# Kernel tuning notes

Hardware: AMD Instinct MI355X
Metric: run time of the kernel (lower is better)

The kernel has to match this reference:

```python
import jax, jax.numpy as jnp
import numpy as np

DIM = 1024


def setup_inputs() -> dict:
    key = jax.random.key(0)
    k1, k2, k3, k4 = jax.random.split(key, 4)
    B, T, S, D = 32, 512, 1024, DIM
    inp = {
        "input": jax.random.normal(k1, (B, T, D), dtype=jnp.float32),
        "context": jax.random.normal(k2, (B, S, D), dtype=jnp.float32),
        # linear_in: nn.Linear(dim, dim, bias=False) -> weight [D, D]
        "W_in": jax.random.normal(k3, (D, D), dtype=jnp.float32) / np.sqrt(D),
        # linear_out: nn.Linear(2*dim, dim, bias=False for 'general') -> weight [D, 2D]
        "W_out": jax.random.normal(k4, (D, 2 * D), dtype=jnp.float32) / np.sqrt(2 * D),
    }
    return inp


def reference(input, context, W_in, W_out):
    # score: general -> h_t = linear_in(input); align = bmm(h_t, context^T)
    h_t = jnp.einsum("btd,ed->bte", input, W_in)              # [B,T,D]
    align = jnp.einsum("btd,bsd->bts", h_t, context)          # [B,T,S]
    align_vectors = jax.nn.softmax(align, axis=-1)            # [B,T,S]
    c = jnp.einsum("bts,bsd->btd", align_vectors, context)    # [B,T,D]
    concat_c = jnp.concatenate([c, input], axis=2)            # [B,T,2D]
    attn_h = jnp.tanh(jnp.einsum("btf,df->btd", concat_c, W_out))  # [B,T,D]
    # multi-step path: transpose to (tgt_len, batch, ...)
    attn_h = jnp.transpose(attn_h, (1, 0, 2))
    concat_c = jnp.transpose(concat_c, (1, 0, 2))
    align_vectors = jnp.transpose(align_vectors, (1, 0, 2))
    return attn_h, align_vectors, concat_c
```

## Files before the change

### kernel.cpp

```cpp
#include <hip/hip_runtime.h>
#include <cmath>

#define BATCH 32
#define TLEN  512
#define SLEN  1024
#define DIM   1024

#define BM 128
#define BN 128
#define BK2 64

typedef _Float16 h8 __attribute__((ext_vector_type(8)));
typedef _Float16 h4 __attribute__((ext_vector_type(4)));
typedef _Float16 h2 __attribute__((ext_vector_type(2)));
typedef float f4 __attribute__((ext_vector_type(4)));


__device__ __forceinline__ void gload16(const _Float16* g, _Float16* l) {
  __builtin_amdgcn_global_load_lds(
      (const __attribute__((address_space(1))) unsigned int*)g,
      (__attribute__((address_space(3))) unsigned int*)l, 16, 0, 0);
}

template <int EPI>
__global__ __launch_bounds__(256) void gemm16(
    const _Float16* __restrict__ A, const _Float16* __restrict__ Bm,
    float* __restrict__ C, _Float16* __restrict__ C16, int K,
    long lda, long ldb, long ldc, long ldc16,
    long strideA, long strideB, long strideC, long strideC16,
    const float* __restrict__ Xin) {
  __shared__ _Float16 As[BM * BK2];
  __shared__ _Float16 Bs[BM * BK2];

  const int bz = blockIdx.z;
  A += (long)bz * strideA;
  Bm += (long)bz * strideB;

  const int m0 = blockIdx.y * BM;
  const int n0 = blockIdx.x * BN;
  const int tid = threadIdx.x;
  const int lane = tid & 63;
  const int wave = tid >> 6;
  const int q = lane >> 4;
  const int r = lane & 15;
  const int wm = (wave >> 1) * 64;
  const int wn = (wave & 1) * 64;

  f4 acc[4][4];
#pragma unroll
  for (int i = 0; i < 4; ++i)
#pragma unroll
    for (int j = 0; j < 4; ++j) acc[i][j] = (f4){0.f, 0.f, 0.f, 0.f};

  const _Float16* gA[4];
  const _Float16* gB[4];
  _Float16* lA[4];
  _Float16* lB[4];
#pragma unroll
  for (int i = 0; i < 4; ++i) {
    const int c = i * 256 + tid;
    const int row = c >> 3;
    const int j = (c & 7) ^ (row & 7);
    gA[i] = A + (long)(m0 + row) * lda + j * 8;
    gB[i] = Bm + (long)(n0 + row) * ldb + j * 8;
    lA[i] = As + i * 2048 + wave * 512;
    lB[i] = Bs + i * 2048 + wave * 512;
  }

  for (int k0 = 0; k0 < K; k0 += BK2) {
#pragma unroll
    for (int i = 0; i < 4; ++i) gload16(gA[i] + k0, lA[i]);
#pragma unroll
    for (int i = 0; i < 4; ++i) gload16(gB[i] + k0, lB[i]);
    __syncthreads();

#pragma unroll
    for (int kk = 0; kk < 2; ++kk) {
      h8 av[4], bv[4];
#pragma unroll
      for (int mt = 0; mt < 4; ++mt) {
        const int row = wm + mt * 16 + r;
        const int u = (kk * 4 + q) ^ (r & 7);
        av[mt] = *(const h8*)&As[row * BK2 + u * 8];
      }
#pragma unroll
      for (int nt = 0; nt < 4; ++nt) {
        const int row = wn + nt * 16 + r;
        const int u = (kk * 4 + q) ^ (r & 7);
        bv[nt] = *(const h8*)&Bs[row * BK2 + u * 8];
      }
#pragma unroll
      for (int mt = 0; mt < 4; ++mt)
#pragma unroll
        for (int nt = 0; nt < 4; ++nt)
          acc[mt][nt] = __builtin_amdgcn_mfma_f32_16x16x32_f16(
              av[mt], bv[nt], acc[mt][nt], 0, 0, 0);
    }
    __syncthreads();
  }

#pragma unroll
  for (int mt = 0; mt < 4; ++mt) {
#pragma unroll
    for (int nt = 0; nt < 4; ++nt) {
#pragma unroll
      for (int i = 0; i < 4; ++i) {
        float x = acc[mt][nt][i];
        const long row = m0 + wm + mt * 16 + q * 4 + i;
        const long col = n0 + wn + nt * 16 + r;
        if constexpr (EPI == 1) x = tanhf(x);
        if constexpr (EPI != 2)
          C[(long)bz * strideC + row * ldc + col] = x;
        if constexpr (EPI >= 2)
          C16[(long)bz * strideC16 + row * ldc16 + col] = (_Float16)x;
      }
    }
  }

  if constexpr (EPI == 4) {
#pragma unroll
    for (int it = 0; it < 16; ++it) {
      const int idx = it * 256 + tid;
      const int row = idx >> 5;
      const int c4 = (idx & 31) * 4;
      const f4 v = *(const f4*)(Xin + ((long)bz * TLEN + m0 + row) * DIM +
                                n0 + c4);
      const long off = (long)bz * strideC + (long)(m0 + row) * ldc + DIM +
                       n0 + c4;
      *(f4*)(C + off) = v;
      h4 hv = {(_Float16)v.x, (_Float16)v.y, (_Float16)v.z, (_Float16)v.w};
      *(h4*)(C16 + (long)bz * strideC16 + (long)(m0 + row) * ldc16 + DIM +
             n0 + c4) = hv;
    }
  }
}

__global__ __launch_bounds__(256) void cvt3(
    const float* __restrict__ in, _Float16* __restrict__ out,
    const float* __restrict__ in2, _Float16* __restrict__ out2,
    const float* __restrict__ in3, _Float16* __restrict__ out3) {
  const int b = blockIdx.x;
  const float* src;
  _Float16* dst;
  long n;
  int b0, nb;
  if (b < 384) { src = in;  dst = out;  n = 16777216; b0 = 0;   nb = 384; }
  else if (b < 408) { src = in2; dst = out2; n = 1048576; b0 = 384; nb = 24; }
  else { src = in3; dst = out3; n = 2097152; b0 = 408; nb = 48; }
  long i = ((long)(b - b0) * 256 + threadIdx.x) * 4;
  const long stride = (long)nb * 1024;
  for (; i < n; i += stride) {
    f4 v = *(const f4*)(src + i);
    h4 hv = {(_Float16)v.x, (_Float16)v.y, (_Float16)v.z, (_Float16)v.w};
    *(h4*)(dst + i) = hv;
  }
}

#define CTPAD 68
__global__ __launch_bounds__(256) void ctx_cvt(
    const float* __restrict__ ctx, _Float16* __restrict__ c16,
    _Float16* __restrict__ c16t) {
  __shared__ _Float16 tile[64 * CTPAD];
  const int b = blockIdx.z;
  const int s0 = blockIdx.y * 64;
  const int d0 = blockIdx.x * 64;
  const int tr = threadIdx.x >> 4;
  const int tc = (threadIdx.x & 15) * 4;
#pragma unroll
  for (int i = 0; i < 4; ++i) {
    const int s = i * 16 + tr;
    float4 v = *(const float4*)(ctx + ((long)b * SLEN + s0 + s) * DIM + d0 + tc);
    h4 hv = {(_Float16)v.x, (_Float16)v.y, (_Float16)v.z, (_Float16)v.w};
    *(h4*)(c16 + ((long)b * SLEN + s0 + s) * DIM + d0 + tc) = hv;
    *(h4*)&tile[s * CTPAD + tc] = hv;
  }
  __syncthreads();
#pragma unroll
  for (int i = 0; i < 4; ++i) {
    const int d = i * 16 + tr;
    h4 hv = {tile[tc * CTPAD + d], tile[(tc + 1) * CTPAD + d],
             tile[(tc + 2) * CTPAD + d], tile[(tc + 3) * CTPAD + d]};
    *(h4*)(c16t + ((long)b * DIM + d0 + d) * SLEN + s0 + tc) = hv;
  }
}


#define AS_LD 40
#define B2_LD 134
#define BKF 32

template <bool B_IS_NT, bool TANH>
__global__ __launch_bounds__(256) void gemm_f16(
    const float* __restrict__ A, const float* __restrict__ Bm,
    float* __restrict__ C, int M, int N, int K, long lda, long ldb, long ldc,
    long strideA, long strideB, long strideC) {
  __shared__ _Float16 As[BM * AS_LD];
  __shared__ _Float16 Bs[BM * AS_LD];

  const int bz = blockIdx.z;
  A += (long)bz * strideA;
  Bm += (long)bz * strideB;
  C += (long)bz * strideC;

  const int m0 = blockIdx.y * BM;
  const int n0 = blockIdx.x * BN;
  const int tid = threadIdx.x;
  const int lane = tid & 63;
  const int wave = tid >> 6;
  const int wm = (wave >> 1) * 64;
  const int wn = (wave & 1) * 64;
  const int q = lane >> 4;
  const int r = lane & 15;

  f4 acc[4][4];
#pragma unroll
  for (int i = 0; i < 4; ++i)
#pragma unroll
    for (int j = 0; j < 4; ++j) acc[i][j] = (f4){0.f, 0.f, 0.f, 0.f};

  const int srow = tid >> 3;
  const int skq = (tid & 7) * 4;
  const int nrow = tid >> 5;
  const int nnq = (tid & 31) * 4;

  for (int k0 = 0; k0 < K; k0 += BKF) {
#pragma unroll
    for (int it = 0; it < 4; ++it) {
      const int row = it * 32 + srow;
      f4 v = *(const f4*)(A + (long)(m0 + row) * lda + k0 + skq);
      h4 hv = {(_Float16)v.x, (_Float16)v.y, (_Float16)v.z, (_Float16)v.w};
      *(h4*)&As[row * AS_LD + skq] = hv;
    }
    if (B_IS_NT) {
#pragma unroll
      for (int it = 0; it < 4; ++it) {
        const int row = it * 32 + srow;
        f4 v = *(const f4*)(Bm + (long)(n0 + row) * ldb + k0 + skq);
        h4 hv = {(_Float16)v.x, (_Float16)v.y, (_Float16)v.z, (_Float16)v.w};
        *(h4*)&Bs[row * AS_LD + skq] = hv;
      }
    } else {
#pragma unroll
      for (int it = 0; it < 4; ++it) {
        const int krow = it * 8 + nrow;
        f4 v = *(const f4*)(Bm + (long)(k0 + krow) * ldb + n0 + nnq);
        _Float16* p = &Bs[krow * B2_LD + nnq];
        *(h2*)p = (h2){(_Float16)v.x, (_Float16)v.y};
        *(h2*)(p + 2) = (h2){(_Float16)v.z, (_Float16)v.w};
      }
    }
    __syncthreads();

    h8 av[4], bv[4];
#pragma unroll
    for (int mt = 0; mt < 4; ++mt)
      av[mt] = *(const h8*)&As[(wm + mt * 16 + r) * AS_LD + q * 8];
    if (B_IS_NT) {
#pragma unroll
      for (int nt = 0; nt < 4; ++nt)
        bv[nt] = *(const h8*)&Bs[(wn + nt * 16 + r) * AS_LD + q * 8];
    } else {
#pragma unroll
      for (int nt = 0; nt < 4; ++nt) {
        h8 t;
#pragma unroll
        for (int j = 0; j < 8; ++j)
          t[j] = Bs[(q * 8 + j) * B2_LD + wn + nt * 16 + r];
        bv[nt] = t;
      }
    }
#pragma unroll
    for (int mt = 0; mt < 4; ++mt)
#pragma unroll
      for (int nt = 0; nt < 4; ++nt)
        acc[mt][nt] = __builtin_amdgcn_mfma_f32_16x16x32_f16(
            av[mt], bv[nt], acc[mt][nt], 0, 0, 0);
    __syncthreads();
  }

#pragma unroll
  for (int mt = 0; mt < 4; ++mt) {
#pragma unroll
    for (int nt = 0; nt < 4; ++nt) {
#pragma unroll
      for (int i = 0; i < 4; ++i) {
        float x = acc[mt][nt][i];
        if (TANH) x = tanhf(x);
        C[(long)(m0 + wm + mt * 16 + q * 4 + i) * ldc + n0 + wn + nt * 16 + r] = x;
      }
    }
  }
}


__global__ __launch_bounds__(256) void softmax_kernel(
    float* __restrict__ data, _Float16* __restrict__ p16) {
  float* row = data + (long)blockIdx.x * SLEN;
  const int tid = threadIdx.x;
  float4 v = ((float4*)row)[tid];
  float m = fmaxf(fmaxf(v.x, v.y), fmaxf(v.z, v.w));
#pragma unroll
  for (int off = 32; off > 0; off >>= 1) m = fmaxf(m, __shfl_xor(m, off));
  __shared__ float redm[4];
  __shared__ float reds[4];
  if ((tid & 63) == 0) redm[tid >> 6] = m;
  __syncthreads();
  m = fmaxf(fmaxf(redm[0], redm[1]), fmaxf(redm[2], redm[3]));
  v.x = expf(v.x - m);
  v.y = expf(v.y - m);
  v.z = expf(v.z - m);
  v.w = expf(v.w - m);
  float s = v.x + v.y + v.z + v.w;
#pragma unroll
  for (int off = 32; off > 0; off >>= 1) s += __shfl_xor(s, off);
  if ((tid & 63) == 0) reds[tid >> 6] = s;
  __syncthreads();
  s = reds[0] + reds[1] + reds[2] + reds[3];
  const float inv = 1.0f / s;
  v.x *= inv;
  v.y *= inv;
  v.z *= inv;
  v.w *= inv;
  ((float4*)row)[tid] = v;
  if (p16) {
    h4 hv = {(_Float16)v.x, (_Float16)v.y, (_Float16)v.z, (_Float16)v.w};
    *(h4*)(p16 + (long)blockIdx.x * SLEN + tid * 4) = hv;
  }
}

__global__ __launch_bounds__(256) void concat_copy_kernel(
    const float* __restrict__ in, float* __restrict__ concat,
    _Float16* __restrict__ c16) {
  const int bt = blockIdx.x;
  const int b = bt >> 9;
  const int t = bt & 511;
  const float4 v = ((const float4*)(in + (long)bt * DIM))[threadIdx.x];
  const long off = ((long)t * BATCH + b) * (2 * DIM) + DIM;
  ((float4*)(concat + off))[threadIdx.x] = v;
  if (c16) {
    h4 hv = {(_Float16)v.x, (_Float16)v.y, (_Float16)v.z, (_Float16)v.w};
    *(h4*)(c16 + off + threadIdx.x * 4) = hv;
  }
}


extern "C" void kernel_launch(void* const* d_in, const int* in_sizes, int n_in,
                              void* d_out, int out_size, void* d_ws,
                              size_t ws_size, hipStream_t stream) {
  const float* input = (const float*)d_in[0];
  const float* context = (const float*)d_in[1];
  const float* W_in = (const float*)d_in[2];
  const float* W_out = (const float*)d_in[3];

  float* out = (float*)d_out;
  float* attn_h = out;
  float* align = out + (long)TLEN * BATCH * DIM;
  float* concat = align + (long)TLEN * BATCH * SLEN;

  const long BT = (long)BATCH * TLEN;
  const long ND = (long)BATCH * TLEN * DIM;

  const size_t WS_NEED = (size_t)3 * 67108864 + 4194304;

  if (d_ws != nullptr && ws_size >= WS_NEED) {
    _Float16* ctx16 = (_Float16*)d_ws;
    _Float16* ctx16t = ctx16 + (long)BATCH * SLEN * DIM;
    _Float16* cat16 = ctx16t + (long)BATCH * SLEN * DIM;
    _Float16* wout16 = cat16 + (long)TLEN * BATCH * 2 * DIM;
    _Float16* in16 = (_Float16*)align;
    _Float16* win16 = in16 + ND;
    _Float16* ht16 = (_Float16*)attn_h;
    _Float16* p16 = ht16 + ND;

    cvt3<<<456, 256, 0, stream>>>(input, in16, W_in, win16, W_out, wout16);
    ctx_cvt<<<dim3(16, 16, BATCH), 256, 0, stream>>>(context, ctx16, ctx16t);

    gemm16<2><<<dim3(DIM / BN, BT / BM, 1), 256, 0, stream>>>(
        in16, win16, nullptr, ht16, DIM,
         DIM,  DIM,  0,  DIM, 0, 0, 0, 0,
        nullptr);

    gemm16<0><<<dim3(SLEN / BN, TLEN / BM, BATCH), 256, 0, stream>>>(
        ht16, ctx16, align, nullptr, DIM,
         DIM,  DIM,  (long)BATCH * SLEN,  0,
         (long)TLEN * DIM,  (long)SLEN * DIM,  SLEN, 0,
        nullptr);

    softmax_kernel<<<(int)BT, 256, 0, stream>>>(align, p16);

    gemm16<4><<<dim3(DIM / BN, TLEN / BM, BATCH), 256, 0, stream>>>(
        p16, ctx16t, concat, cat16, SLEN,
         (long)BATCH * SLEN,  SLEN,
         (long)BATCH * 2 * DIM,  (long)BATCH * 2 * DIM,
         SLEN,  (long)DIM * SLEN,  2 * DIM,
         2 * DIM, input);

    gemm16<1><<<dim3(DIM / BN, BT / BM, 1), 256, 0, stream>>>(
        cat16, wout16, attn_h, nullptr, 2 * DIM,
         2 * DIM,  2 * DIM,  DIM,  0, 0, 0, 0, 0,
        nullptr);
    return;
  }

  float* h_t = attn_h;

  gemm_f16<true, false><<<dim3(DIM / BN, BT / BM, 1), 256, 0, stream>>>(
      input, W_in, h_t, (int)BT, DIM, DIM, DIM, DIM, DIM, 0, 0, 0);

  gemm_f16<true, false><<<dim3(SLEN / BN, TLEN / BM, BATCH), 256, 0, stream>>>(
      h_t, context, align, TLEN, SLEN, DIM, DIM, DIM, (long)BATCH * SLEN,
      (long)TLEN * DIM, (long)SLEN * DIM, SLEN);

  softmax_kernel<<<(int)BT, 256, 0, stream>>>(align, nullptr);

  gemm_f16<false, false><<<dim3(DIM / BN, TLEN / BM, BATCH), 256, 0, stream>>>(
      align, context, concat, TLEN, DIM, SLEN, (long)BATCH * SLEN, DIM,
      (long)BATCH * 2 * DIM, SLEN, (long)SLEN * DIM, 2 * DIM);

  concat_copy_kernel<<<(int)BT, 256, 0, stream>>>(input, concat, nullptr);

  gemm_f16<true, true><<<dim3(DIM / BN, BT / BM, 1), 256, 0, stream>>>(
      concat, W_out, attn_h, (int)BT, DIM, 2 * DIM, 2 * DIM, 2 * DIM, DIM,
      0, 0, 0);
}
```

Measured before the change: 765.4 us.

## Replace 128x128 fp16 GEMM with double-buffered 256x256 8-wave pipelined kernel

Replaces the single-buffered 128x128 tile GEMM with a 256x256 tile, 512-thread kernel. It double-buffers LDS and stages the next K-tile's A and B halves with global_load_lds, interleaved between four MFMA quadrant phases. Explicit sched barriers, s_barrier, waitcnt and setprio are used to overlap memory with compute and to raise arithmetic intensity per tile. The cost is a larger LDS footprint (128KB) and more accumulator registers. It also fragments the work into fewer blocks, which may hurt occupancy on the smaller GEMMs.

```diff
diff --git a/kernel.cpp b/kernel.cpp
--- a/kernel.cpp
+++ b/kernel.cpp
@@ -6,108 +6,188 @@
 #define SLEN  1024
 #define DIM   1024
 
-#define BM 128
-#define BN 128
-#define BK2 64
-
 typedef _Float16 h8 __attribute__((ext_vector_type(8)));
 typedef _Float16 h4 __attribute__((ext_vector_type(4)));
 typedef _Float16 h2 __attribute__((ext_vector_type(2)));
 typedef float f4 __attribute__((ext_vector_type(4)));
 
-
 __device__ __forceinline__ void gload16(const _Float16* g, _Float16* l) {
   __builtin_amdgcn_global_load_lds(
       (const __attribute__((address_space(1))) unsigned int*)g,
       (__attribute__((address_space(3))) unsigned int*)l, 16, 0, 0);
 }
 
+
+__device__ __forceinline__ void stage_half(
+    const _Float16* __restrict__ g, long ld, int k0,
+    _Float16* lds_region, int wave, int lane) {
+#pragma unroll
+  for (int i = 0; i < 2; ++i) {
+    const int c = (i * 8 + wave) * 64 + lane;
+    const int rl = c >> 3;
+    const int j = (c & 7) ^ (rl & 7);
+    gload16(g + (long)rl * ld + k0 + j * 8,
+            lds_region + (i * 8 + wave) * 512);
+  }
+}
+
+#define SFENCE __builtin_amdgcn_sched_barrier(0)
+#define SBAR   __builtin_amdgcn_s_barrier()
+
 template <int EPI>
-__global__ __launch_bounds__(256) void gemm16(
+__global__ __launch_bounds__(512, 2) void gemm256(
     const _Float16* __restrict__ A, const _Float16* __restrict__ Bm,
     float* __restrict__ C, _Float16* __restrict__ C16, int K,
     long lda, long ldb, long ldc, long ldc16,
     long strideA, long strideB, long strideC, long strideC16,
     const float* __restrict__ Xin) {
-  __shared__ _Float16 As[BM * BK2];
-  __shared__ _Float16 Bs[BM * BK2];
+  __shared__ _Float16 LA[2][256][64];
+  __shared__ _Float16 LB[2][256][64];
 
   const int bz = blockIdx.z;
   A += (long)bz * strideA;
   Bm += (long)bz * strideB;
 
-  const int m0 = blockIdx.y * BM;
-  const int n0 = blockIdx.x * BN;
+  const int m0 = blockIdx.y * 256;
+  const int n0 = blockIdx.x * 256;
   const int tid = threadIdx.x;
   const int lane = tid & 63;
   const int wave = tid >> 6;
+  const int wr = wave >> 2;
+  const int wc = wave & 3;
   const int q = lane >> 4;
   const int r = lane & 15;
-  const int wm = (wave >> 1) * 64;
-  const int wn = (wave & 1) * 64;
-
-  f4 acc[4][4];
-#pragma unroll
-  for (int i = 0; i < 4; ++i)
+
+  f4 acc[8][4];
+#pragma unroll
+  for (int i = 0; i < 8; ++i)
 #pragma unroll
     for (int j = 0; j < 4; ++j) acc[i][j] = (f4){0.f, 0.f, 0.f, 0.f};
 
-  const _Float16* gA[4];
-  const _Float16* gB[4];
-  _Float16* lA[4];
-  _Float16* lB[4];
-#pragma unroll
-  for (int i = 0; i < 4; ++i) {
-    const int c = i * 256 + tid;
-    const int row = c >> 3;
-    const int j = (c & 7) ^ (row & 7);
-    gA[i] = A + (long)(m0 + row) * lda + j * 8;
-    gB[i] = Bm + (long)(n0 + row) * ldb + j * 8;
-    lA[i] = As + i * 2048 + wave * 512;
-    lB[i] = Bs + i * 2048 + wave * 512;
-  }
-
-  for (int k0 = 0; k0 < K; k0 += BK2) {
-#pragma unroll
-    for (int i = 0; i < 4; ++i) gload16(gA[i] + k0, lA[i]);
-#pragma unroll
-    for (int i = 0; i < 4; ++i) gload16(gB[i] + k0, lB[i]);
-    __syncthreads();
-
-#pragma unroll
-    for (int kk = 0; kk < 2; ++kk) {
-      h8 av[4], bv[4];
-#pragma unroll
-      for (int mt = 0; mt < 4; ++mt) {
-        const int row = wm + mt * 16 + r;
-        const int u = (kk * 4 + q) ^ (r & 7);
-        av[mt] = *(const h8*)&As[row * BK2 + u * 8];
-      }
-#pragma unroll
-      for (int nt = 0; nt < 4; ++nt) {
-        const int row = wn + nt * 16 + r;
-        const int u = (kk * 4 + q) ^ (r & 7);
-        bv[nt] = *(const h8*)&Bs[row * BK2 + u * 8];
-      }
-#pragma unroll
-      for (int mt = 0; mt < 4; ++mt)
-#pragma unroll
-        for (int nt = 0; nt < 4; ++nt)
-          acc[mt][nt] = __builtin_amdgcn_mfma_f32_16x16x32_f16(
-              av[mt], bv[nt], acc[mt][nt], 0, 0, 0);
-    }
-    __syncthreads();
-  }
-
-#pragma unroll
-  for (int mt = 0; mt < 4; ++mt) {
+  const int ntile = K >> 6;
+
+  stage_half(A + (long)m0 * lda, lda, 0, &LA[0][0][0], wave, lane);
+  stage_half(A + (long)(m0 + 128) * lda, lda, 0, &LA[0][128][0], wave, lane);
+  stage_half(Bm + (long)n0 * ldb, ldb, 0, &LB[0][0][0], wave, lane);
+  stage_half(Bm + (long)(n0 + 128) * ldb, ldb, 0, &LB[0][128][0], wave, lane);
+  if (ntile > 1) {
+    stage_half(Bm + (long)n0 * ldb, ldb, 64, &LB[1][0][0], wave, lane);
+    stage_half(Bm + (long)(n0 + 128) * ldb, ldb, 64, &LB[1][128][0], wave, lane);
+    stage_half(A + (long)m0 * lda, lda, 64, &LA[1][0][0], wave, lane);
+    asm volatile("s_waitcnt vmcnt(6)" ::: "memory");
+  } else {
+    asm volatile("s_waitcnt vmcnt(0)" ::: "memory");
+  }
+  SBAR;
+
+  for (int t = 0; t < ntile; ++t) {
+    const int p = t & 1;
+    const bool s1 = (t + 1) < ntile;
+    const bool s2 = (t + 2) < ntile;
+    const int k1 = (t + 1) << 6;
+    const int k2 = (t + 2) << 6;
+
+    h8 a_lo[4][2], a_hi[4][2], b[4][2];
+
+#pragma unroll
+    for (int mt = 0; mt < 4; ++mt)
+#pragma unroll
+      for (int kk = 0; kk < 2; ++kk)
+        a_lo[mt][kk] = *(const h8*)&LA[p][wr * 128 + mt * 16 + r]
+                                      [((kk * 4 + q) ^ (r & 7)) * 8];
+#pragma unroll
+    for (int nn = 0; nn < 4; ++nn)
+#pragma unroll
+      for (int kk = 0; kk < 2; ++kk)
+        b[nn][kk] = *(const h8*)&LB[p][wc * 64 + nn * 16 + r]
+                                     [((kk * 4 + q) ^ (r & 7)) * 8];
+    if (s1)
+      stage_half(A + (long)(m0 + 128) * lda, lda, k1, &LA[p ^ 1][128][0],
+                 wave, lane);
+    SFENCE; SBAR;
+    asm volatile("s_waitcnt lgkmcnt(0)" ::: "memory");
+    SFENCE;
+    __builtin_amdgcn_s_setprio(1);
+#pragma unroll
+    for (int mt = 0; mt < 4; ++mt)
+#pragma unroll
+      for (int nn = 0; nn < 2; ++nn)
+#pragma unroll
+        for (int kk = 0; kk < 2; ++kk)
+          acc[mt][nn] = __builtin_amdgcn_mfma_f32_16x16x32_f16(
+              a_lo[mt][kk], b[nn][kk], acc[mt][nn], 0, 0, 0);
+    __builtin_amdgcn_s_setprio(0);
+    SFENCE; SBAR;
+
+#pragma unroll
+    for (int mt = 0; mt < 4; ++mt)
+#pragma unroll
+      for (int kk = 0; kk < 2; ++kk)
+        a_hi[mt][kk] = *(const h8*)&LA[p][wr * 128 + 64 + mt * 16 + r]
+                                       [((kk * 4 + q) ^ (r & 7)) * 8];
+    if (s2) stage_half(Bm + (long)n0 * ldb, ldb, k2, &LB[p][0][0], wave, lane);
+    SFENCE; SBAR;
+    asm volatile("s_waitcnt lgkmcnt(0)" ::: "memory");
+    SFENCE;
+    __builtin_amdgcn_s_setprio(1);
+#pragma unroll
+    for (int mt = 0; mt < 4; ++mt)
+#pragma unroll
+      for (int nn = 0; nn < 2; ++nn)
+#pragma unroll
+        for (int kk = 0; kk < 2; ++kk)
+          acc[mt][2 + nn] = __builtin_amdgcn_mfma_f32_16x16x32_f16(
+              a_lo[mt][kk], b[2 + nn][kk], acc[mt][2 + nn], 0, 0, 0);
+    __builtin_amdgcn_s_setprio(0);
+    SFENCE; SBAR;
+
+    if (s2)
+      stage_half(Bm + (long)(n0 + 128) * ldb, ldb, k2, &LB[p][128][0],
+                 wave, lane);
+    SFENCE; SBAR;
+    asm volatile("s_waitcnt lgkmcnt(0)" ::: "memory");
+    SFENCE;
+    __builtin_amdgcn_s_setprio(1);
+#pragma unroll
+    for (int mt = 0; mt < 4; ++mt)
+#pragma unroll
+      for (int nn = 0; nn < 2; ++nn)
+#pragma unroll
+        for (int kk = 0; kk < 2; ++kk)
+          acc[4 + mt][nn] = __builtin_amdgcn_mfma_f32_16x16x32_f16(
+              a_hi[mt][kk], b[nn][kk], acc[4 + mt][nn], 0, 0, 0);
+    __builtin_amdgcn_s_setprio(0);
+    SFENCE; SBAR;
+
+    if (s2) stage_half(A + (long)m0 * lda, lda, k2, &LA[p][0][0], wave, lane);
+    SFENCE; SBAR;
+    asm volatile("s_waitcnt lgkmcnt(0)" ::: "memory");
+    SFENCE;
+    __builtin_amdgcn_s_setprio(1);
+#pragma unroll
+    for (int mt = 0; mt < 4; ++mt)
+#pragma unroll
+      for (int nn = 0; nn < 2; ++nn)
+#pragma unroll
+        for (int kk = 0; kk < 2; ++kk)
+          acc[4 + mt][2 + nn] = __builtin_amdgcn_mfma_f32_16x16x32_f16(
+              a_hi[mt][kk], b[2 + nn][kk], acc[4 + mt][2 + nn], 0, 0, 0);
+    __builtin_amdgcn_s_setprio(0);
+    SFENCE;
+    if (s2) asm volatile("s_waitcnt vmcnt(6)" ::: "memory");
+    else    asm volatile("s_waitcnt vmcnt(0)" ::: "memory");
+    SBAR;
+  }
+
+#pragma unroll
+  for (int mt = 0; mt < 8; ++mt) {
 #pragma unroll
     for (int nt = 0; nt < 4; ++nt) {
 #pragma unroll
       for (int i = 0; i < 4; ++i) {
         float x = acc[mt][nt][i];
-        const long row = m0 + wm + mt * 16 + q * 4 + i;
-        const long col = n0 + wn + nt * 16 + r;
+        const long row = m0 + wr * 128 + mt * 16 + q * 4 + i;
+        const long col = n0 + wc * 64 + nt * 16 + r;
         if constexpr (EPI == 1) x = tanhf(x);
         if constexpr (EPI != 2)
           C[(long)bz * strideC + row * ldc + col] = x;
@@ -119,15 +199,14 @@
 
   if constexpr (EPI == 4) {
 #pragma unroll
-    for (int it = 0; it < 16; ++it) {
-      const int idx = it * 256 + tid;
-      const int row = idx >> 5;
-      const int c4 = (idx & 31) * 4;
+    for (int it = 0; it < 32; ++it) {
+      const int idx = it * 512 + tid;
+      const int row = idx >> 6;
+      const int c4 = (idx & 63) * 4;
       const f4 v = *(const f4*)(Xin + ((long)bz * TLEN + m0 + row) * DIM +
                                 n0 + c4);
-      const long off = (long)bz * strideC + (long)(m0 + row) * ldc + DIM +
-                       n0 + c4;
-      *(f4*)(C + off) = v;
+      *(f4*)(C + (long)bz * strideC + (long)(m0 + row) * ldc + DIM + n0 + c4) =
+          v;
       h4 hv = {(_Float16)v.x, (_Float16)v.y, (_Float16)v.z, (_Float16)v.w};
       *(h4*)(C16 + (long)bz * strideC16 + (long)(m0 + row) * ldc16 + DIM +
              n0 + c4) = hv;
@@ -185,6 +264,7 @@
 }
 
 
+#define FBM 128
 #define AS_LD 40
 #define B2_LD 134
 #define BKF 32
@@ -194,16 +274,16 @@
     const float* __restrict__ A, const float* __restrict__ Bm,
     float* __restrict__ C, int M, int N, int K, long lda, long ldb, long ldc,
     long strideA, long strideB, long strideC) {
-  __shared__ _Float16 As[BM * AS_LD];
-  __shared__ _Float16 Bs[BM * AS_LD];
+  __shared__ _Float16 As[FBM * AS_LD];
+  __shared__ _Float16 Bs[FBM * AS_LD];
 
   const int bz = blockIdx.z;
   A += (long)bz * strideA;
   Bm += (long)bz * strideB;
   C += (long)bz * strideC;
 
-  const int m0 = blockIdx.y * BM;
-  const int n0 = blockIdx.x * BN;
+  const int m0 = blockIdx.y * FBM;
+  const int n0 = blockIdx.x * FBM;
   const int tid = threadIdx.x;
   const int lane = tid & 63;
   const int wave = tid >> 6;
@@ -262,11 +342,11 @@
     } else {
 #pragma unroll
       for (int nt = 0; nt < 4; ++nt) {
-        h8 t;
+        h8 tv;
 #pragma unroll
         for (int j = 0; j < 8; ++j)
-          t[j] = Bs[(q * 8 + j) * B2_LD + wn + nt * 16 + r];
-        bv[nt] = t;
+          tv[j] = Bs[(q * 8 + j) * B2_LD + wn + nt * 16 + r];
+        bv[nt] = tv;
       }
     }
 #pragma unroll
@@ -375,12 +455,12 @@
     cvt3<<<456, 256, 0, stream>>>(input, in16, W_in, win16, W_out, wout16);
     ctx_cvt<<<dim3(16, 16, BATCH), 256, 0, stream>>>(context, ctx16, ctx16t);
 
-    gemm16<2><<<dim3(DIM / BN, BT / BM, 1), 256, 0, stream>>>(
+    gemm256<2><<<dim3(DIM / 256, BT / 256, 1), 512, 0, stream>>>(
         in16, win16, nullptr, ht16, DIM,
          DIM,  DIM,  0,  DIM, 0, 0, 0, 0,
         nullptr);
 
-    gemm16<0><<<dim3(SLEN / BN, TLEN / BM, BATCH), 256, 0, stream>>>(
+    gemm256<0><<<dim3(SLEN / 256, TLEN / 256, BATCH), 512, 0, stream>>>(
         ht16, ctx16, align, nullptr, DIM,
          DIM,  DIM,  (long)BATCH * SLEN,  0,
          (long)TLEN * DIM,  (long)SLEN * DIM,  SLEN, 0,
@@ -388,14 +468,14 @@
 
     softmax_kernel<<<(int)BT, 256, 0, stream>>>(align, p16);
 
-    gemm16<4><<<dim3(DIM / BN, TLEN / BM, BATCH), 256, 0, stream>>>(
+    gemm256<4><<<dim3(DIM / 256, TLEN / 256, BATCH), 512, 0, stream>>>(
         p16, ctx16t, concat, cat16, SLEN,
          (long)BATCH * SLEN,  SLEN,
          (long)BATCH * 2 * DIM,  (long)BATCH * 2 * DIM,
          SLEN,  (long)DIM * SLEN,  2 * DIM,
          2 * DIM, input);
 
-    gemm16<1><<<dim3(DIM / BN, BT / BM, 1), 256, 0, stream>>>(
+    gemm256<1><<<dim3(DIM / 256, BT / 256, 1), 512, 0, stream>>>(
         cat16, wout16, attn_h, nullptr, 2 * DIM,
          2 * DIM,  2 * DIM,  DIM,  0, 0, 0, 0, 0,
         nullptr);
@@ -404,22 +484,22 @@
 
   float* h_t = attn_h;
 
-  gemm_f16<true, false><<<dim3(DIM / BN, BT / BM, 1), 256, 0, stream>>>(
+  gemm_f16<true, false><<<dim3(DIM / FBM, BT / FBM, 1), 256, 0, stream>>>(
       input, W_in, h_t, (int)BT, DIM, DIM, DIM, DIM, DIM, 0, 0, 0);
 
-  gemm_f16<true, false><<<dim3(SLEN / BN, TLEN / BM, BATCH), 256, 0, stream>>>(
+  gemm_f16<true, false><<<dim3(SLEN / FBM, TLEN / FBM, BATCH), 256, 0, stream>>>(
       h_t, context, align, TLEN, SLEN, DIM, DIM, DIM, (long)BATCH * SLEN,
       (long)TLEN * DIM, (long)SLEN * DIM, SLEN);
 
   softmax_kernel<<<(int)BT, 256, 0, stream>>>(align, nullptr);
 
-  gemm_f16<false, false><<<dim3(DIM / BN, TLEN / BM, BATCH), 256, 0, stream>>>(
+  gemm_f16<false, false><<<dim3(DIM / FBM, TLEN / FBM, BATCH), 256, 0, stream>>>(
       align, context, concat, TLEN, DIM, SLEN, (long)BATCH * SLEN, DIM,
       (long)BATCH * 2 * DIM, SLEN, (long)SLEN * DIM, 2 * DIM);
 
   concat_copy_kernel<<<(int)BT, 256, 0, stream>>>(input, concat, nullptr);
 
-  gemm_f16<true, true><<<dim3(DIM / BN, BT / BM, 1), 256, 0, stream>>>(
+  gemm_f16<true, true><<<dim3(DIM / FBM, BT / FBM, 1), 256, 0, stream>>>(
       concat, W_out, attn_h, (int)BT, DIM, 2 * DIM, 2 * DIM, 2 * DIM, DIM,
       0, 0, 0);
 }
```

Result: faster. 710.5 us (-7.2%).
